# Optimization experiments

Hardware: AMD Instinct MI355X
Metric: run time of the kernel (lower is better)

The kernel has to match this reference:

```python
import jax, jax.numpy as jnp
import numpy as np

B, D, E, H, OUT = 4096, 1024, 8, 4096, 1024


def setup_inputs() -> dict:
    key = jax.random.key(0)
    ks = jax.random.split(key, 8)
    s_in = 1.0 / np.sqrt(D)
    s_h = 1.0 / np.sqrt(H)
    return {
        "x": jax.random.normal(ks[0], (B, D), dtype=jnp.float32),
        "Wg": jax.random.uniform(ks[1], (D, E), minval=-s_in, maxval=s_in, dtype=jnp.float32),
        "bg": jnp.zeros((E,), dtype=jnp.float32),
        "W1": jax.random.uniform(ks[2], (E, D, H), minval=-s_in, maxval=s_in, dtype=jnp.float32),
        "b1": jnp.zeros((E, H), dtype=jnp.float32),
        "W2": jax.random.uniform(ks[3], (E, H, OUT), minval=-s_h, maxval=s_h, dtype=jnp.float32),
        "b2": jnp.zeros((E, OUT), dtype=jnp.float32),
        "w_bal": jnp.float32(0.01),
    }


def reference(x, Wg, bg, W1, b1, W2, b2, w_bal):
    # Gating: softmax then top-1 (== argmax of logits)
    gate_logits = x @ Wg + bg                      # [B, E]
    assign = jnp.argmax(gate_logits, axis=1)       # [B] top-1 expert
    onehot = jax.nn.one_hot(assign, E, dtype=x.dtype)  # [B, E] dispatch mask

    # Dense dispatch: run every expert MLP, combine by one-hot (top-1 select).
    # Original returns raw expert output (no gate-prob scaling).
    h = jax.nn.relu(jnp.einsum("bd,edh->ebh", x, W1) + b1[:, None, :])  # [E, B, H]
    y = jnp.einsum("ebh,eho->ebo", h, W2) + b2[:, None, :]              # [E, B, OUT]
    output = jnp.einsum("ebo,be->bo", y, onehot)                        # [B, OUT]

    # Load-balance loss on per-expert token counts
    loads = onehot.sum(axis=0)                     # [E]
    balance_loss = jnp.sum((loads - loads.mean()) ** 2) / E
    return output, balance_loss * w_bal
```

## Files before the change

### kernel.cpp

```cpp
#include <hip/hip_runtime.h>
#include <hip/hip_bf16.h>

typedef unsigned short u16;
typedef __attribute__((ext_vector_type(8))) short bf16x8;
typedef __attribute__((ext_vector_type(4))) float f32x4;

#define BTOK 4096
#define DDIM 1024
#define NEXP 8
#define HDIM 4096
#define ODIM 1024
#define MAXT 23
#define MROWS (MAXT * 256)

__device__ __forceinline__ u16 f2bf(float f) {
  unsigned u = __float_as_uint(f);
  return (u16)((u + 0x7FFFu + ((u >> 16) & 1u)) >> 16);
}
__device__ __forceinline__ u16 cvt_bf(float f) {
  __hip_bfloat16 h = __float2bfloat16(f);
  u16 r;
  __builtin_memcpy(&r, &h, 2);
  return r;
}
__device__ __forceinline__ void gload16(const void* g, void* l) {
  __builtin_amdgcn_global_load_lds(
      (const __attribute__((address_space(1))) void*)g,
      (__attribute__((address_space(3))) void*)l, 16, 0, 0);
}

#define SFENCE __builtin_amdgcn_sched_barrier(0)
#define SBAR                        \
  do {                              \
    SFENCE;                         \
    __builtin_amdgcn_s_barrier();   \
    SFENCE;                         \
  } while (0)

__global__ __launch_bounds__(256) void init_kernel(int* __restrict__ ctrl,
                                                   int* __restrict__ rowmap) {
  int i = blockIdx.x * 256 + threadIdx.x;
  if (i < 1024)
    ctrl[i] = 0;
  else
    rowmap[i - 1024] = -1;
}

__global__ __launch_bounds__(256) void gate_kernel(
    const float* __restrict__ x, const float* __restrict__ Wg,
    const float* __restrict__ bg, int* __restrict__ assign,
    int* __restrict__ counts) {
  int wave = threadIdx.x >> 6;
  int lane = threadIdx.x & 63;
  int b = blockIdx.x * 4 + wave;
  const float* xr = x + (size_t)b * DDIM;
  double acc[NEXP];
#pragma unroll
  for (int e = 0; e < NEXP; ++e) acc[e] = 0.0;
  for (int d = lane; d < DDIM; d += 64) {
    float xv = xr[d];
    const float4* wrow = (const float4*)(Wg + d * NEXP);
    float4 w0 = wrow[0], w1 = wrow[1];
    acc[0] += (double)xv * (double)w0.x;
    acc[1] += (double)xv * (double)w0.y;
    acc[2] += (double)xv * (double)w0.z;
    acc[3] += (double)xv * (double)w0.w;
    acc[4] += (double)xv * (double)w1.x;
    acc[5] += (double)xv * (double)w1.y;
    acc[6] += (double)xv * (double)w1.z;
    acc[7] += (double)xv * (double)w1.w;
  }
#pragma unroll
  for (int e = 0; e < NEXP; ++e) {
    double v = acc[e];
#pragma unroll
    for (int off = 32; off > 0; off >>= 1) v += __shfl_xor(v, off);
    acc[e] = v;
  }
  if (lane == 0) {
    int best = 0;
    double bv = acc[0] + (double)bg[0];
#pragma unroll
    for (int e = 1; e < NEXP; ++e) {
      double v = acc[e] + (double)bg[e];
      if (v > bv) { bv = v; best = e; }
    }
    assign[b] = best;
    atomicAdd(&counts[best], 1);
  }
}

__global__ void setup_kernel(const int* __restrict__ counts,
                             const float* __restrict__ wbal,
                             int* __restrict__ offp, int* __restrict__ tile_e,
                             int* __restrict__ tile_m, int* __restrict__ meta,
                             float* __restrict__ loss_out) {
  if (threadIdx.x != 0 || blockIdx.x != 0) return;
  int off = 0, nt = 0;
  for (int e = 0; e < NEXP; ++e) {
    offp[e] = off;
    int pc = (counts[e] + 255) & ~255;
    for (int t = 0; t < (pc >> 8); ++t) {
      tile_e[nt] = e;
      tile_m[nt] = off + t * 256;
      ++nt;
    }
    off += pc;
  }
  offp[NEXP] = off;
  meta[0] = nt;
  float mean = (float)BTOK / (float)NEXP;
  float s = 0.f;
  for (int e = 0; e < NEXP; ++e) {
    float d = (float)counts[e] - mean;
    s += d * d;
  }
  loss_out[0] = s / (float)NEXP * wbal[0];
}

__global__ __launch_bounds__(256) void gather_kernel(
    const float* __restrict__ x, const int* __restrict__ assign,
    const int* __restrict__ offp, int* __restrict__ fill,
    int* __restrict__ rowmap, u16* __restrict__ xg) {
  int b = blockIdx.x;
  __shared__ int srow;
  if (threadIdx.x == 0) {
    int e = assign[b];
    int pos = atomicAdd(&fill[e], 1);
    int row = offp[e] + pos;
    rowmap[row] = b;
    srow = row;
  }
  __syncthreads();
  int row = srow;
  float4 v = *(const float4*)(x + (size_t)b * DDIM + threadIdx.x * 4);
  ushort4 o;
  o.x = f2bf(v.x);
  o.y = f2bf(v.y);
  o.z = f2bf(v.z);
  o.w = f2bf(v.w);
  *(ushort4*)(xg + (size_t)row * DDIM + threadIdx.x * 4) = o;
}

__global__ __launch_bounds__(256) void transpose_conv(
    const float* __restrict__ W, u16* __restrict__ wt, int N, int K) {
  const int e = blockIdx.z;
  const int kb = blockIdx.x * 256, nb = blockIdx.y * 64;
  __shared__ __align__(16) float lds[256][66];
  const float* src = W + (size_t)e * K * N;
  const int t = threadIdx.x;
  const int rr = t >> 4, cc = (t & 15) * 4;
#pragma unroll
  for (int p = 0; p < 16; ++p) {
    float4 v =
        *(const float4*)(src + (size_t)(kb + rr + p * 16) * N + nb + cc);
    *(float4*)&lds[rr + p * 16][cc] = v;
  }
  __syncthreads();
  const int n = t & 63, kg = (t >> 6) * 64;
  alignas(16) u16 tmp[64];
#pragma unroll
  for (int i = 0; i < 64; ++i) tmp[i] = cvt_bf(lds[kg + i][n]);
  u16* dst = wt + ((size_t)e * N + nb + n) * K + kb + kg;
#pragma unroll
  for (int q = 0; q < 8; ++q) *(float4*)(dst + q * 8) = *(float4*)&tmp[q * 8];
}

template <int MODE>
__device__ __forceinline__ void gemm8p_core(
    char* lds, int bx, int by, int bz, const u16* __restrict__ A, int lda,
    const u16* __restrict__ BT, int ldb, int nbRows,
    const float* __restrict__ bias, const int* __restrict__ tile_e,
    const int* __restrict__ tile_m, u16* __restrict__ Hout, int ldn,
    float* __restrict__ P, size_t pStride, int NT, int kOff) {
  const int e = tile_e[bx];
  const int m0 = tile_m[bx];
  const int n0 = by * 256;

  const int tid = threadIdx.x;
  const int lane = tid & 63;
  const int wid = tid >> 6;
  const int wr = wid >> 2;
  const int wc = wid & 3;
  const int fr = lane & 15;
  const int kqr = lane >> 4;

  const int rS = tid >> 3, gS = tid & 7;
  const int koctOff = (gS ^ (rS & 7)) * 8;
  const u16* aB0 = A + (size_t)(m0 + rS) * lda + kOff + koctOff;
  const u16* bB0 = BT + ((size_t)e * nbRows + n0 + rS) * ldb + kOff + koctOff;

  auto stageA = [&](int kt, int half) {
    char* dst = lds + (kt & 1) * 65536 + half * 16384 + tid * 16;
    const u16* s = aB0 + (size_t)(half * 128) * lda + kt * 64;
    gload16(s, dst);
    gload16(s + (size_t)64 * lda, dst + 8192);
  };
  auto stageB = [&](int kt, int half) {
    char* dst = lds + (kt & 1) * 65536 + 32768 + half * 16384 + tid * 16;
    const u16* s = bB0 + (size_t)(half * 128) * ldb + kt * 64;
    gload16(s, dst);
    gload16(s + (size_t)64 * ldb, dst + 8192);
  };

  int aOff[4][2], bOff[2][2];
#pragma unroll
  for (int mi = 0; mi < 4; ++mi) {
    int r = wr * 64 + mi * 16 + fr;
#pragma unroll
    for (int ks = 0; ks < 2; ++ks)
      aOff[mi][ks] = r * 128 + (((ks * 4 + kqr) ^ (r & 7)) * 16);
  }
#pragma unroll
  for (int ni = 0; ni < 2; ++ni) {
    int c = wc * 32 + ni * 16 + fr;
#pragma unroll
    for (int ks = 0; ks < 2; ++ks)
      bOff[ni][ks] = c * 128 + (((ks * 4 + kqr) ^ (c & 7)) * 16);
  }

  f32x4 acc[8][4];
#pragma unroll
  for (int i = 0; i < 8; ++i)
#pragma unroll
    for (int j = 0; j < 4; ++j)
#pragma unroll
      for (int r = 0; r < 4; ++r) acc[i][j][r] = 0.f;

  bf16x8 af[4][2], bA[2][2], bB[2][2];

  auto ldA = [&](int dB, int mq) {
    const char* rg = lds + dB + mq * 16384;
#pragma unroll
    for (int mi = 0; mi < 4; ++mi)
#pragma unroll
      for (int ks = 0; ks < 2; ++ks)
        af[mi][ks] = *(const bf16x8*)(rg + aOff[mi][ks]);
  };
  auto ldB = [&](int dB, int nq, bf16x8 (&bf)[2][2]) {
    const char* rg = lds + dB + 32768 + nq * 16384;
#pragma unroll
    for (int ni = 0; ni < 2; ++ni)
#pragma unroll
      for (int ks = 0; ks < 2; ++ks)
        bf[ni][ks] = *(const bf16x8*)(rg + bOff[ni][ks]);
  };
  auto MM = [&](int mq, int nq, bf16x8 (&bf)[2][2]) {
    __builtin_amdgcn_s_setprio(1);
#pragma unroll
    for (int ks = 0; ks < 2; ++ks)
#pragma unroll
      for (int mi = 0; mi < 4; ++mi)
#pragma unroll
        for (int ni = 0; ni < 2; ++ni)
          acc[mq * 4 + mi][nq * 2 + ni] = __builtin_amdgcn_mfma_f32_16x16x32_bf16(
              af[mi][ks], bf[ni][ks], acc[mq * 4 + mi][nq * 2 + ni], 0, 0, 0);
    __builtin_amdgcn_s_setprio(0);
  };

  stageA(0, 0);
  stageB(0, 0);
  stageA(0, 1);
  stageB(0, 1);
  stageA(1, 0);
  stageB(1, 0);
  asm volatile("s_waitcnt vmcnt(8)" ::: "memory");
  SBAR;

  const int NI = NT >> 1;
#pragma unroll 1
  for (int i = 0; i < NI; ++i) {
    const int kt1 = 2 * i + 1, kt2 = 2 * i + 2, kt3 = 2 * i + 3;
    const bool more = (i + 1 < NI);
    ldA(0, 0);
    ldB(0, 0, bA);
    stageA(kt1, 1);
    SBAR;
    asm volatile("s_waitcnt lgkmcnt(0)" ::: "memory");
    SFENCE;
    MM(0, 0, bA);
    asm volatile("s_waitcnt vmcnt(6)" ::: "memory");
    SBAR;
    ldB(0, 1, bB);
    stageB(kt1, 1);
    SBAR;
    asm volatile("s_waitcnt lgkmcnt(0)" ::: "memory");
    SFENCE;
    MM(0, 1, bB);
    SBAR;
    ldA(0, 1);
    if (more) stageA(kt2, 0);
    SBAR;
    asm volatile("s_waitcnt lgkmcnt(0)" ::: "memory");
    SFENCE;
    MM(1, 0, bA);
    SBAR;
    if (more) stageB(kt2, 0);
    SBAR;
    MM(1, 1, bB);
    if (more)
      asm volatile("s_waitcnt vmcnt(8)" ::: "memory");
    else
      asm volatile("s_waitcnt vmcnt(0)" ::: "memory");
    SBAR;
    ldA(65536, 0);
    ldB(65536, 0, bA);
    if (more) stageA(kt2, 1);
    SBAR;
    asm volatile("s_waitcnt lgkmcnt(0)" ::: "memory");
    SFENCE;
    MM(0, 0, bA);
    if (more) asm volatile("s_waitcnt vmcnt(6)" ::: "memory");
    SBAR;
    ldB(65536, 1, bB);
    if (more) stageB(kt2, 1);
    SBAR;
    asm volatile("s_waitcnt lgkmcnt(0)" ::: "memory");
    SFENCE;
    MM(0, 1, bB);
    SBAR;
    ldA(65536, 1);
    if (more) stageA(kt3, 0);
    SBAR;
    asm volatile("s_waitcnt lgkmcnt(0)" ::: "memory");
    SFENCE;
    MM(1, 0, bA);
    SBAR;
    if (more) stageB(kt3, 0);
    SBAR;
    MM(1, 1, bB);
    if (more) asm volatile("s_waitcnt vmcnt(8)" ::: "memory");
    SBAR;
  }

#pragma unroll
  for (int mq = 0; mq < 2; ++mq)
#pragma unroll
    for (int mi = 0; mi < 4; ++mi) {
      const int rbase = m0 + mq * 128 + wr * 64 + mi * 16 + (lane >> 4) * 4;
#pragma unroll
      for (int nq = 0; nq < 2; ++nq)
#pragma unroll
        for (int ni = 0; ni < 2; ++ni) {
          const int col = n0 + nq * 128 + wc * 32 + ni * 16 + fr;
          const f32x4 a = acc[mq * 4 + mi][nq * 2 + ni];
          if constexpr (MODE == 0) {
            const float bv = bias[e * ldn + col];
#pragma unroll
            for (int r = 0; r < 4; ++r) {
              float v = a[r] + bv;
              v = v > 0.f ? v : 0.f;
              Hout[(size_t)(rbase + r) * ldn + col] = f2bf(v);
            }
          } else {
            float* Pp = P + bz * pStride;
#pragma unroll
            for (int r = 0; r < 4; ++r)
              Pp[(size_t)(rbase + r) * ODIM + col] = a[r];
          }
        }
    }
}

__global__ __launch_bounds__(512, 2) void moe_gemm1(
    const u16* __restrict__ xg, const u16* __restrict__ wt1,
    const float* __restrict__ b1, const int* __restrict__ tile_e,
    const int* __restrict__ tile_m, const int* __restrict__ meta,
    u16* __restrict__ h) {
  __shared__ __align__(16) char lds[131072];
  const int orig = blockIdx.y * MAXT + blockIdx.x;
  const int xcd = orig & 7;
  const int idx = orig >> 3;
  const int by = xcd * 2 + idx / MAXT;
  const int bx = idx % MAXT;
  if (bx >= meta[0]) return;
  gemm8p_core<0>(lds, bx, by, 0, xg, DDIM, wt1, DDIM, HDIM, b1, tile_e,
                 tile_m, h, HDIM, nullptr, 0, DDIM / 64, 0);
}

__global__ __launch_bounds__(512, 2) void moe_gemm2(
    const u16* __restrict__ h, const u16* __restrict__ wt2,
    const int* __restrict__ tile_e, const int* __restrict__ tile_m,
    const int* __restrict__ meta, float* __restrict__ P, size_t pStride) {
  __shared__ __align__(16) char lds[131072];
  const int orig = (blockIdx.z * 4 + blockIdx.y) * MAXT + blockIdx.x;
  const int xcd = orig & 7;
  const int idx = orig >> 3;
  const int wg = xcd * MAXT + idx;
  const int z = wg / 92;
  const int rem = wg % 92;
  const int by = rem / MAXT;
  const int bx = rem % MAXT;
  if (bx >= meta[0]) return;
  gemm8p_core<1>(lds, bx, by, z, h, HDIM, wt2, HDIM, ODIM, nullptr, tile_e,
                 tile_m, nullptr, 0, P, pStride, 32, z * 2048);
}

__global__ __launch_bounds__(256) void reduce_kernel(
    const float* __restrict__ P, size_t pStride, const int* __restrict__ rowmap,
    const int* __restrict__ tile_e, const int* __restrict__ tile_m,
    const int* __restrict__ meta, const float* __restrict__ b2,
    float* __restrict__ out) {
  if ((int)blockIdx.x >= meta[0]) return;
  const int e = tile_e[blockIdx.x];
  const int m0 = tile_m[blockIdx.x];
  const int c0 = blockIdx.y * 128;
#pragma unroll 1
  for (int it = 0; it < 32; ++it) {
    int idx = it * 256 + threadIdx.x;
    int r = idx >> 5, cq = idx & 31;
    int row = m0 + r;
    int tok = rowmap[row];
    if (tok < 0) continue;
    int c = c0 + cq * 4;
    float4 a = *(const float4*)(P + (size_t)row * ODIM + c);
    float4 b = *(const float4*)(P + pStride + (size_t)row * ODIM + c);
    float4 bb = *(const float4*)(b2 + (size_t)e * ODIM + c);
    float4 o;
    o.x = a.x + b.x + bb.x;
    o.y = a.y + b.y + bb.y;
    o.z = a.z + b.z + bb.z;
    o.w = a.w + b.w + bb.w;
    *(float4*)(out + (size_t)tok * ODIM + c) = o;
  }
}

extern "C" void kernel_launch(void* const* d_in, const int* in_sizes, int n_in,
                              void* d_out, int out_size, void* d_ws,
                              size_t ws_size, hipStream_t stream) {
  const float* x = (const float*)d_in[0];
  const float* Wg = (const float*)d_in[1];
  const float* bg = (const float*)d_in[2];
  const float* W1 = (const float*)d_in[3];
  const float* b1 = (const float*)d_in[4];
  const float* W2 = (const float*)d_in[5];
  const float* b2 = (const float*)d_in[6];
  const float* wbal = (const float*)d_in[7];
  float* out = (float*)d_out;

  char* ws = (char*)d_ws;
  int* counts = (int*)(ws + 0);
  int* fill = (int*)(ws + 64);
  int* offp = (int*)(ws + 128);
  int* meta = (int*)(ws + 192);
  int* tile_e = (int*)(ws + 256);
  int* tile_m = (int*)(ws + 512);
  int* assign = (int*)(ws + 4096);
  int* rowmap = (int*)(ws + 20480);
  u16* xg = (u16*)(ws + 65536);
  u16* h = (u16*)(ws + 12582912);
  float* P = (float*)(ws + 61865984);
  u16* wt1 = (u16*)(ws + 110100480);
  u16* wt2 = (u16*)(ws + 177209344);
  const size_t pStride = (size_t)MROWS * ODIM;

  init_kernel<<<27, 256, 0, stream>>>((int*)ws, rowmap);
  gate_kernel<<<BTOK / 4, 256, 0, stream>>>(x, Wg, bg, assign, counts);
  setup_kernel<<<1, 64, 0, stream>>>(counts, wbal, offp, tile_e, tile_m, meta,
                                     out + (size_t)BTOK * ODIM);
  gather_kernel<<<BTOK, 256, 0, stream>>>(x, assign, offp, fill, rowmap, xg);

  transpose_conv<<<dim3(DDIM / 256, HDIM / 64, NEXP), 256, 0, stream>>>(
      W1, wt1, HDIM, DDIM);
  transpose_conv<<<dim3(HDIM / 256, ODIM / 64, NEXP), 256, 0, stream>>>(
      W2, wt2, ODIM, HDIM);

  moe_gemm1<<<dim3(MAXT, HDIM / 256), 512, 0, stream>>>(
      xg, wt1, b1, tile_e, tile_m, meta, h);
  moe_gemm2<<<dim3(MAXT, ODIM / 256, 2), 512, 0, stream>>>(
      h, wt2, tile_e, tile_m, meta, P, pStride);
  reduce_kernel<<<dim3(MAXT, ODIM / 128), 256, 0, stream>>>(
      P, pStride, rowmap, tile_e, tile_m, meta, b2, out);
}
```

Before: 352.4 us.

## Fuse split-K reduction into gemm2 via atomic adds and shrink transpose LDS

The second GEMM now atomically accumulates its split-K partial results, plus the bias on the first split, straight into the token-ordered output. This removes the partial-sum buffer and the separate reduce kernel. The init kernel is widened so it zeroes the output first. The weight transpose converts to bf16 before staging in a smaller LDS tile processed in two halves, which lowers LDS use. Atomics add contention and make summation order nondeterministic, and zeroing the output adds write traffic.

```diff
diff --git a/kernel.cpp b/kernel.cpp
--- a/kernel.cpp
+++ b/kernel.cpp
@@ -38,12 +38,20 @@
   } while (0)
 
 __global__ __launch_bounds__(256) void init_kernel(int* __restrict__ ctrl,
-                                                   int* __restrict__ rowmap) {
+                                                   int* __restrict__ rowmap,
+                                                   float* __restrict__ out) {
   int i = blockIdx.x * 256 + threadIdx.x;
-  if (i < 1024)
-    ctrl[i] = 0;
-  else
-    rowmap[i - 1024] = -1;
+  if (i < 524288) {
+    float4 z = make_float4(0.f, 0.f, 0.f, 0.f);
+    *(float4*)(out + (size_t)i * 8) = z;
+    *(float4*)(out + (size_t)i * 8 + 4) = z;
+  } else {
+    int j = i - 524288;
+    if (j < 1024)
+      ctrl[j] = 0;
+    else if (j < 1024 + MROWS)
+      rowmap[j - 1024] = -1;
+  }
 }
 
 __global__ __launch_bounds__(256) void gate_kernel(
@@ -146,24 +154,42 @@
     const float* __restrict__ W, u16* __restrict__ wt, int N, int K) {
   const int e = blockIdx.z;
   const int kb = blockIdx.x * 256, nb = blockIdx.y * 64;
-  __shared__ __align__(16) float lds[256][66];
+  __shared__ __align__(16) u16 lds[2][128][72];
   const float* src = W + (size_t)e * K * N;
   const int t = threadIdx.x;
   const int rr = t >> 4, cc = (t & 15) * 4;
-#pragma unroll
-  for (int p = 0; p < 16; ++p) {
-    float4 v =
-        *(const float4*)(src + (size_t)(kb + rr + p * 16) * N + nb + cc);
-    *(float4*)&lds[rr + p * 16][cc] = v;
-  }
-  __syncthreads();
-  const int n = t & 63, kg = (t >> 6) * 64;
-  alignas(16) u16 tmp[64];
-#pragma unroll
-  for (int i = 0; i < 64; ++i) tmp[i] = cvt_bf(lds[kg + i][n]);
-  u16* dst = wt + ((size_t)e * N + nb + n) * K + kb + kg;
-#pragma unroll
-  for (int q = 0; q < 8; ++q) *(float4*)(dst + q * 8) = *(float4*)&tmp[q * 8];
+
+  float4 v0[8], v1[8];
+#pragma unroll
+  for (int p = 0; p < 8; ++p)
+    v0[p] = *(const float4*)(src + (size_t)(kb + rr + p * 16) * N + nb + cc);
+#pragma unroll
+  for (int p = 0; p < 8; ++p)
+    v1[p] =
+        *(const float4*)(src + (size_t)(kb + 128 + rr + p * 16) * N + nb + cc);
+
+  const int n = t & 63, kg = (t >> 6) * 32;
+#pragma unroll
+  for (int h = 0; h < 2; ++h) {
+#pragma unroll
+    for (int p = 0; p < 8; ++p) {
+      float4 v = h == 0 ? v0[p] : v1[p];
+      ushort4 o;
+      o.x = cvt_bf(v.x);
+      o.y = cvt_bf(v.y);
+      o.z = cvt_bf(v.z);
+      o.w = cvt_bf(v.w);
+      *(ushort4*)&lds[h][rr + p * 16][cc] = o;
+    }
+    __syncthreads();
+    alignas(16) u16 tmp[32];
+#pragma unroll
+    for (int i = 0; i < 32; ++i) tmp[i] = lds[h][kg + i][n];
+    u16* dst = wt + ((size_t)e * N + nb + n) * K + kb + h * 128 + kg;
+#pragma unroll
+    for (int q = 0; q < 4; ++q) *(float4*)(dst + q * 8) = *(float4*)&tmp[q * 8];
+    if (h == 0) __syncthreads();
+  }
 }
 
 template <int MODE>
@@ -171,8 +197,9 @@
     char* lds, int bx, int by, int bz, const u16* __restrict__ A, int lda,
     const u16* __restrict__ BT, int ldb, int nbRows,
     const float* __restrict__ bias, const int* __restrict__ tile_e,
-    const int* __restrict__ tile_m, u16* __restrict__ Hout, int ldn,
-    float* __restrict__ P, size_t pStride, int NT, int kOff) {
+    const int* __restrict__ tile_m, const int* __restrict__ rowmap,
+    u16* __restrict__ Hout, int ldn, float* __restrict__ Cout, int NT,
+    int kOff) {
   const int e = tile_e[bx];
   const int m0 = tile_m[bx];
   const int n0 = by * 256;
@@ -338,6 +365,11 @@
 #pragma unroll
     for (int mi = 0; mi < 4; ++mi) {
       const int rbase = m0 + mq * 128 + wr * 64 + mi * 16 + (lane >> 4) * 4;
+      int tok[4];
+      if constexpr (MODE == 1) {
+#pragma unroll
+        for (int r = 0; r < 4; ++r) tok[r] = rowmap[rbase + r];
+      }
 #pragma unroll
       for (int nq = 0; nq < 2; ++nq)
 #pragma unroll
@@ -353,10 +385,12 @@
               Hout[(size_t)(rbase + r) * ldn + col] = f2bf(v);
             }
           } else {
-            float* Pp = P + bz * pStride;
-#pragma unroll
-            for (int r = 0; r < 4; ++r)
-              Pp[(size_t)(rbase + r) * ODIM + col] = a[r];
+            const float bv = (bz == 0) ? bias[e * ldn + col] : 0.f;
+#pragma unroll
+            for (int r = 0; r < 4; ++r) {
+              if (tok[r] >= 0)
+                unsafeAtomicAdd(&Cout[(size_t)tok[r] * ODIM + col], a[r] + bv);
+            }
           }
         }
     }
@@ -375,13 +409,14 @@
   const int bx = idx % MAXT;
   if (bx >= meta[0]) return;
   gemm8p_core<0>(lds, bx, by, 0, xg, DDIM, wt1, DDIM, HDIM, b1, tile_e,
-                 tile_m, h, HDIM, nullptr, 0, DDIM / 64, 0);
+                 tile_m, nullptr, h, HDIM, nullptr, DDIM / 64, 0);
 }
 
 __global__ __launch_bounds__(512, 2) void moe_gemm2(
     const u16* __restrict__ h, const u16* __restrict__ wt2,
-    const int* __restrict__ tile_e, const int* __restrict__ tile_m,
-    const int* __restrict__ meta, float* __restrict__ P, size_t pStride) {
+    const float* __restrict__ b2, const int* __restrict__ tile_e,
+    const int* __restrict__ tile_m, const int* __restrict__ meta,
+    const int* __restrict__ rowmap, float* __restrict__ out) {
   __shared__ __align__(16) char lds[131072];
   const int orig = (blockIdx.z * 4 + blockIdx.y) * MAXT + blockIdx.x;
   const int xcd = orig & 7;
@@ -392,37 +427,8 @@
   const int by = rem / MAXT;
   const int bx = rem % MAXT;
   if (bx >= meta[0]) return;
-  gemm8p_core<1>(lds, bx, by, z, h, HDIM, wt2, HDIM, ODIM, nullptr, tile_e,
-                 tile_m, nullptr, 0, P, pStride, 32, z * 2048);
-}
-
-__global__ __launch_bounds__(256) void reduce_kernel(
-    const float* __restrict__ P, size_t pStride, const int* __restrict__ rowmap,
-    const int* __restrict__ tile_e, const int* __restrict__ tile_m,
-    const int* __restrict__ meta, const float* __restrict__ b2,
-    float* __restrict__ out) {
-  if ((int)blockIdx.x >= meta[0]) return;
-  const int e = tile_e[blockIdx.x];
-  const int m0 = tile_m[blockIdx.x];
-  const int c0 = blockIdx.y * 128;
-#pragma unroll 1
-  for (int it = 0; it < 32; ++it) {
-    int idx = it * 256 + threadIdx.x;
-    int r = idx >> 5, cq = idx & 31;
-    int row = m0 + r;
-    int tok = rowmap[row];
-    if (tok < 0) continue;
-    int c = c0 + cq * 4;
-    float4 a = *(const float4*)(P + (size_t)row * ODIM + c);
-    float4 b = *(const float4*)(P + pStride + (size_t)row * ODIM + c);
-    float4 bb = *(const float4*)(b2 + (size_t)e * ODIM + c);
-    float4 o;
-    o.x = a.x + b.x + bb.x;
-    o.y = a.y + b.y + bb.y;
-    o.z = a.z + b.z + bb.z;
-    o.w = a.w + b.w + bb.w;
-    *(float4*)(out + (size_t)tok * ODIM + c) = o;
-  }
+  gemm8p_core<1>(lds, bx, by, z, h, HDIM, wt2, HDIM, ODIM, b2, tile_e, tile_m,
+                 rowmap, nullptr, ODIM, out, 32, z * 2048);
 }
 
 extern "C" void kernel_launch(void* const* d_in, const int* in_sizes, int n_in,
@@ -449,12 +455,10 @@
   int* rowmap = (int*)(ws + 20480);
   u16* xg = (u16*)(ws + 65536);
   u16* h = (u16*)(ws + 12582912);
-  float* P = (float*)(ws + 61865984);
   u16* wt1 = (u16*)(ws + 110100480);
   u16* wt2 = (u16*)(ws + 177209344);
-  const size_t pStride = (size_t)MROWS * ODIM;
-
-  init_kernel<<<27, 256, 0, stream>>>((int*)ws, rowmap);
+
+  init_kernel<<<2075, 256, 0, stream>>>((int*)ws, rowmap, out);
   gate_kernel<<<BTOK / 4, 256, 0, stream>>>(x, Wg, bg, assign, counts);
   setup_kernel<<<1, 64, 0, stream>>>(counts, wbal, offp, tile_e, tile_m, meta,
                                      out + (size_t)BTOK * ODIM);
@@ -468,7 +472,5 @@
   moe_gemm1<<<dim3(MAXT, HDIM / 256), 512, 0, stream>>>(
       xg, wt1, b1, tile_e, tile_m, meta, h);
   moe_gemm2<<<dim3(MAXT, ODIM / 256, 2), 512, 0, stream>>>(
-      h, wt2, tile_e, tile_m, meta, P, pStride);
-  reduce_kernel<<<dim3(MAXT, ODIM / 128), 256, 0, stream>>>(
-      P, pStride, rowmap, tile_e, tile_m, meta, b2, out);
-}
+      h, wt2, b2, tile_e, tile_m, meta, rowmap, out);
+}
```

Measured after the change: 380.7 us. 1.08x slower.
